# Kernel tuning notes

Measured on AMD Instinct MI355X. Metric: run time of the kernel, lower is better.

Reference implementation:

```python
import math
import jax, jax.numpy as jnp
import numpy as np

B, T, C, HS = 4, 4096, 1024, 64  # batch, seq, n_embd, head_size=n_embd//n_head

def setup_inputs() -> dict:
    key = jax.random.key(0)
    k0, k1, k2, k3 = jax.random.split(key, 4)
    x = jax.random.normal(k0, (B, T, C), dtype=jnp.float32)
    Wq = jax.random.normal(k1, (C, HS), dtype=jnp.float32) * 0.02
    Wk = jax.random.normal(k2, (C, HS), dtype=jnp.float32) * 0.02
    Wv = jax.random.normal(k3, (C, HS), dtype=jnp.float32) * 0.02
    return {"x": x, "Wq": Wq, "Wk": Wk, "Wv": Wv}

def reference(x, Wq, Wk, Wv):
    b, t, c = x.shape
    q = x @ Wq                                   # [B,T,hs]
    k = x @ Wk                                   # [B,T,hs]
    v = x @ Wv                                   # [B,T,hs]
    wei = jnp.einsum('btd,bsd->bts', q, k)       # [B,T,T] raw scores
    row_sums = wei.sum(axis=-1)                  # [B,T]
    k_sel = math.ceil(t / 2)                     # static: t known at trace time
    _, idx = jax.lax.top_k(row_sums, k_sel)      # [B,k_sel]
    idx = jnp.sort(idx, axis=1)
    # gather selected score rows: [B,k_sel,T]
    half_wei = jnp.take_along_axis(wei, idx[:, :, None], axis=1)
    # causal mask rows gathered from tril: tril[idx[b,i], j] == (j <= idx[b,i])
    half_mask = jnp.arange(t)[None, None, :] <= idx[:, :, None]  # [B,k_sel,T] bool
    half_wei = half_wei * (c ** -0.5)            # NOTE: scaled by n_embd, as in source
    half_wei = jnp.where(half_mask, half_wei, -jnp.inf)
    att = jax.nn.softmax(half_wei, axis=-1)      # [B,k_sel,T]
    out = att @ v                                # [B,k_sel,hs]
    return out
```

## Files before the change

kernel.cpp:

```cpp
#include <hip/hip_runtime.h>
#include <math.h>

#define BB 4
#define TT 4096
#define CC 1024
#define HS 64
#define KSEL 2048
#define NSPL 16
#define SWLOG 8
#define SW 256

typedef float f32x4 __attribute__((ext_vector_type(4)));
typedef short short8 __attribute__((ext_vector_type(8)));

__device__ __forceinline__ unsigned short f2bf(float f) {
  union { float f; unsigned int u; } c;
  c.f = f;
  const unsigned int u = c.u;
  return (unsigned short)((u + 0x7FFFu + ((u >> 16) & 1u)) >> 16);
}

__device__ __forceinline__ unsigned cvtpk(float lo, float hi) {
  unsigned r;
  asm("v_cvt_pk_bf16_f32 %0, %1, %2" : "=v"(r) : "v"(lo), "v"(hi));
  return r;
}

__global__ __launch_bounds__(256) void conv_w(const float* __restrict__ Wq,
                                              const float* __restrict__ Wk,
                                              const float* __restrict__ Wv,
                                              unsigned short* __restrict__ wbf,
                                              float* __restrict__ xsum) {
  const int gid = blockIdx.x * 256 + threadIdx.x;
  if (gid < 1024) ((float4*)xsum)[gid] = make_float4(0.f, 0.f, 0.f, 0.f);
  const int kt = gid / 768;
  const int rem = gid - kt * 768;
  const int nt = rem >> 6, lane = rem & 63;
  const int col = nt * 16 + (lane & 15);
  const float* W = (col < 64) ? Wq : ((col < 128) ? Wk : Wv);
  const int cl = col & 63;
  const int k0 = kt * 32 + (lane >> 4) * 8;
  unsigned short tmp[8];
#pragma unroll
  for (int i = 0; i < 8; i++) tmp[i] = f2bf(W[(size_t)(k0 + i) * HS + cl]);
  uint4 o;
  o.x = tmp[0] | ((unsigned)tmp[1] << 16);
  o.y = tmp[2] | ((unsigned)tmp[3] << 16);
  o.z = tmp[4] | ((unsigned)tmp[5] << 16);
  o.w = tmp[6] | ((unsigned)tmp[7] << 16);
  *(uint4*)(wbf + (size_t)gid * 8) = o;
}

#define PR 32
__global__ __launch_bounds__(256) void fusedproj(
    const float* __restrict__ x, const unsigned short* __restrict__ wbf,
    float* __restrict__ xsum, unsigned short* __restrict__ qbf,
    unsigned short* __restrict__ kbf, unsigned short* __restrict__ vtbf) {
  __shared__ unsigned short Xs[PR][256];
  __shared__ float xsred[4][256];
  const int rb = blockIdx.x;
  const size_t r0 = (size_t)rb * PR;
  const int tid = threadIdx.x;
  const int wid = tid >> 6, lane = tid & 63;
  const int lhi = lane >> 4, llo = lane & 15;
  const int mt = wid >> 1, nh = wid & 1;
  const int cl = tid & 63, rg = tid >> 6;
  const int bidx = rb >> 7;

  f32x4 acc[6];
#pragma unroll
  for (int n = 0; n < 6; n++) acc[n] = (f32x4){0.f, 0.f, 0.f, 0.f};

  float4 pf[8];
#pragma unroll
  for (int rr = 0; rr < 8; rr++)
    pf[rr] = *(const float4*)(x + (r0 + rg * 8 + rr) * CC + cl * 4);

  for (int ch = 0; ch < 4; ch++) {
    float ps0 = 0.f, ps1 = 0.f, ps2 = 0.f, ps3 = 0.f;
#pragma unroll
    for (int rr = 0; rr < 8; rr++) {
      const int row = rg * 8 + rr;
      float4 v = pf[rr];
      ps0 += v.x; ps1 += v.y; ps2 += v.z; ps3 += v.w;
      *(uint2*)((char*)&Xs[0][0] + row * 512 +
                ((((cl >> 1) ^ (row & 7))) << 4) + ((cl & 1) << 3)) =
          make_uint2(cvtpk(v.x, v.y), cvtpk(v.z, v.w));
    }
    xsred[rg][cl * 4 + 0] = ps0;
    xsred[rg][cl * 4 + 1] = ps1;
    xsred[rg][cl * 4 + 2] = ps2;
    xsred[rg][cl * 4 + 3] = ps3;
    __syncthreads();
    if (ch < 3) {
#pragma unroll
      for (int rr = 0; rr < 8; rr++)
        pf[rr] = *(const float4*)(x + (r0 + rg * 8 + rr) * CC +
                                  (ch + 1) * 256 + cl * 4);
    }
    atomicAdd(&xsum[bidx * CC + ch * 256 + tid],
              xsred[0][tid] + xsred[1][tid] + xsred[2][tid] + xsred[3][tid]);
    const int row = mt * 16 + llo;
#pragma unroll
    for (int ktl = 0; ktl < 8; ktl++) {
      short8 af = *(const short8*)((const char*)&Xs[0][0] + row * 512 +
                                   ((((ktl << 2) + lhi) ^ (row & 7)) << 4));
      const unsigned short* bp =
          wbf + (((size_t)(ch * 8 + ktl) * 12 + nh * 6) * 64 + lane) * 8;
#pragma unroll
      for (int n = 0; n < 6; n++) {
        short8 bf = *(const short8*)(bp + n * 64 * 8);
        acc[n] = __builtin_amdgcn_mfma_f32_16x16x32_bf16(af, bf, acc[n], 0, 0, 0);
      }
    }
    __syncthreads();
  }
  const int rbg = (int)r0 + mt * 16 + lhi * 4;
#pragma unroll
  for (int n = 0; n < 6; n++) {
    const int col = (nh * 6 + n) * 16 + llo;
    const int mat = col >> 6, cl2 = col & 63;
    if (mat == 0) {
#pragma unroll
      for (int r = 0; r < 4; r++)
        qbf[(size_t)(rbg + r) * HS + cl2] = f2bf(acc[n][r] * 0.03125f);
    } else if (mat == 1) {
#pragma unroll
      for (int r = 0; r < 4; r++)
        kbf[(size_t)(rbg + r) * HS + cl2] = f2bf(acc[n][r]);
    } else {
      const int bb = rbg >> 12, tloc = rbg & (TT - 1);
      *(uint2*)(vtbf + ((size_t)bb * HS + cl2) * TT + tloc) =
          make_uint2(cvtpk(acc[n][0], acc[n][1]), cvtpk(acc[n][2], acc[n][3]));
    }
  }
}

__global__ __launch_bounds__(512) void rowsums_x(
    const float* __restrict__ x, const float* __restrict__ Wq,
    const float* __restrict__ Wk, const float* __restrict__ xsum,
    float* __restrict__ rs) {
  __shared__ float xsl[CC];
  __shared__ float kred[8][HS];
  __shared__ float ksl[HS];
  __shared__ float wl[CC];
  const int g = blockIdx.x;
  const int tid = threadIdx.x;
  const int b = g >> 6;
  *(float2*)(xsl + tid * 2) = *(const float2*)(xsum + b * CC + tid * 2);
  __syncthreads();
  {
    const int g8 = tid >> 6, d = tid & 63;
    const float* wkp = Wk + (size_t)(g8 * 128) * HS + d;
    float s = 0.f;
    for (int c = 0; c < 128; c++) s += xsl[g8 * 128 + c] * wkp[(size_t)c * HS];
    kred[g8][d] = s;
  }
  __syncthreads();
  if (tid < 64) {
    float s = 0.f;
#pragma unroll
    for (int g8 = 0; g8 < 8; g8++) s += kred[g8][tid];
    ksl[tid] = s;
  }
  __syncthreads();
#pragma unroll
  for (int p = 0; p < 2; p++) {
    const int c = tid * 2 + p;
    const float* wqp = Wq + (size_t)c * HS;
    float s = 0.f;
#pragma unroll
    for (int d4 = 0; d4 < 16; d4++) {
      float4 a = *(const float4*)(wqp + d4 * 4);
      float4 kk = *(const float4*)(ksl + d4 * 4);
      s += a.x * kk.x + a.y * kk.y + a.z * kk.z + a.w * kk.w;
    }
    wl[c] = s;
  }
  __syncthreads();
  const size_t row = (size_t)g * 64 + (tid >> 3);
  const int qu = tid & 7;
  const float* xr = x + row * CC + qu * 128;
  const float* wr = wl + qu * 128;
  float s = 0.f;
  for (int e = 0; e < 32; e++) {
    float4 v = *(const float4*)(xr + e * 4);
    float4 w4 = *(const float4*)(wr + e * 4);
    s += v.x * w4.x + v.y * w4.y + v.z * w4.z + v.w * w4.w;
  }
  s += __shfl_xor(s, 1);
  s += __shfl_xor(s, 2);
  s += __shfl_xor(s, 4);
  if (qu == 0) rs[row] = s;
}

__global__ __launch_bounds__(256) void rankk(const float* __restrict__ rs,
                                             int* __restrict__ flag) {
  __shared__ float rl[TT];
  const int g = blockIdx.x;
  const int b = g >> 7, chunk = g & 127;
  const int tid = threadIdx.x;
  const float* rsb = rs + (size_t)b * TT;
  for (int e = tid; e < TT / 4; e += 256)
    *(float4*)(rl + e * 4) = *(const float4*)(rsb + e * 4);
  __syncthreads();
  const int cand = tid >> 3, qu = tid & 7;
  const int t = chunk * 32 + cand;
  const float my = rl[t];
  int cnt = 0;
  for (int e = 0; e < 128; e++) {
    const int s = qu * 512 + e * 4;
    float4 v = *(const float4*)(rl + s);
    cnt += (v.x > my) || (v.x == my && (s + 0) < t);
    cnt += (v.y > my) || (v.y == my && (s + 1) < t);
    cnt += (v.z > my) || (v.z == my && (s + 2) < t);
    cnt += (v.w > my) || (v.w == my && (s + 3) < t);
  }
  cnt += __shfl_xor(cnt, 1);
  cnt += __shfl_xor(cnt, 2);
  cnt += __shfl_xor(cnt, 4);
  if (qu == 0) flag[(size_t)b * TT + t] = (cnt < KSEL) ? 1 : 0;
}

__global__ __launch_bounds__(256) void compact(const int* __restrict__ flag,
                                               int* __restrict__ idx) {
  __shared__ int wsum[4];
  __shared__ int woff[4];
  const int b = blockIdx.x;
  const int tid = threadIdx.x;
  const int wid = tid >> 6, lane = tid & 63;
  const int* fb = flag + (size_t)b * TT;
  const int base = tid * 16;
  int f[16];
  int cnt = 0;
#pragma unroll
  for (int e4 = 0; e4 < 4; e4++) {
    int4 v = *(const int4*)(fb + base + e4 * 4);
    f[e4 * 4 + 0] = v.x; f[e4 * 4 + 1] = v.y;
    f[e4 * 4 + 2] = v.z; f[e4 * 4 + 3] = v.w;
    cnt += v.x + v.y + v.z + v.w;
  }
  int sc = cnt;
#pragma unroll
  for (int d = 1; d < 64; d <<= 1) {
    int v = __shfl_up(sc, d);
    if (lane >= d) sc += v;
  }
  if (lane == 63) wsum[wid] = sc;
  __syncthreads();
  if (tid == 0) {
    int a = 0;
#pragma unroll
    for (int w = 0; w < 4; w++) { woff[w] = a; a += wsum[w]; }
  }
  __syncthreads();
  int pos = woff[wid] + sc - cnt;
#pragma unroll
  for (int e = 0; e < 16; e++)
    if (f[e]) idx[(size_t)b * KSEL + (pos++)] = base + e;
}

struct KF { short8 a0, a1, b0, b1; };
struct VF { short8 v0, v1, v2, v3; };

__global__ __launch_bounds__(256) void attn_mfma(
    const unsigned short* __restrict__ qbf,
    const unsigned short* __restrict__ kbf,
    const unsigned short* __restrict__ vtbf, const int* __restrict__ idx,
    float* __restrict__ pl, float* __restrict__ pacc) {
  __shared__ unsigned short P_lds[4][32][40];
  const int rb = blockIdx.x;
  const int zz = blockIdx.y;
  const int b = blockIdx.z;
  const int tid = threadIdx.x;
  const int wid = tid >> 6, lane = tid & 63;
  const int s = zz * 4 + wid;
  const size_t rbase = (size_t)b * KSEL + rb * 32;
  const int tmaxblk = idx[rbase + 31];
  const int jlo = s << SWLOG;
  if (jlo > tmaxblk) return;

  const int lhi = lane >> 4, llo = lane & 15;
  const int trow0 = idx[rbase + llo];
  const int trow1 = idx[rbase + 16 + llo];
  short8 qf[2][2];
  {
    const unsigned short* qp0 = qbf + ((size_t)b * TT + trow0) * HS + lhi * 8;
    const unsigned short* qp1 = qbf + ((size_t)b * TT + trow1) * HS + lhi * 8;
    qf[0][0] = *(const short8*)(qp0);
    qf[0][1] = *(const short8*)(qp0 + 32);
    qf[1][0] = *(const short8*)(qp1);
    qf[1][1] = *(const short8*)(qp1 + 32);
  }
  f32x4 o[2][4];
#pragma unroll
  for (int mtt = 0; mtt < 2; mtt++)
#pragma unroll
    for (int n = 0; n < 4; n++) o[mtt][n] = (f32x4){0.f, 0.f, 0.f, 0.f};
  float lsum[2] = {0.f, 0.f};

  const unsigned short* kb = kbf + (size_t)b * TT * HS;
  const unsigned short* vb = vtbf + (size_t)b * HS * TT;
  const int jend = min(tmaxblk + 1, jlo + SW);

  auto loadK = [&](int j0) {
    KF K;
    const unsigned short* kp = kb + (size_t)(j0 + llo) * HS + lhi * 8;
    K.a0 = *(const short8*)(kp);
    K.a1 = *(const short8*)(kp + 32);
    K.b0 = *(const short8*)(kp + 16 * HS);
    K.b1 = *(const short8*)(kp + 16 * HS + 32);
    return K;
  };
  auto loadV = [&](int j0) {
    VF V;
    const unsigned short* vp = vb + (size_t)llo * TT + j0 + lhi * 8;
    V.v0 = *(const short8*)(vp);
    V.v1 = *(const short8*)(vp + 16 * TT);
    V.v2 = *(const short8*)(vp + 32 * TT);
    V.v3 = *(const short8*)(vp + 48 * TT);
    return V;
  };

  auto body = [&](int j0, const KF& K, const VF& V) {
    f32x4 sc[2][2];
#pragma unroll
    for (int mtt = 0; mtt < 2; mtt++) {
      f32x4 a = (f32x4){0.f, 0.f, 0.f, 0.f};
      a = __builtin_amdgcn_mfma_f32_16x16x32_bf16(K.a0, qf[mtt][0], a, 0, 0, 0);
      a = __builtin_amdgcn_mfma_f32_16x16x32_bf16(K.a1, qf[mtt][1], a, 0, 0, 0);
      sc[mtt][0] = a;
      f32x4 c = (f32x4){0.f, 0.f, 0.f, 0.f};
      c = __builtin_amdgcn_mfma_f32_16x16x32_bf16(K.b0, qf[mtt][0], c, 0, 0, 0);
      c = __builtin_amdgcn_mfma_f32_16x16x32_bf16(K.b1, qf[mtt][1], c, 0, 0, 0);
      sc[mtt][1] = c;
    }
#pragma unroll
    for (int mtt = 0; mtt < 2; mtt++) {
      const int tr = (mtt == 0) ? trow0 : trow1;
      float p[8];
#pragma unroll
      for (int kt = 0; kt < 2; kt++)
#pragma unroll
        for (int r = 0; r < 4; r++) {
          const int kk = j0 + kt * 16 + lhi * 4 + r;
          const float e = __expf(sc[mtt][kt][r]);
          p[kt * 4 + r] = (kk <= tr) ? e : 0.f;
        }
      lsum[mtt] += ((p[0] + p[1]) + (p[2] + p[3])) +
                   ((p[4] + p[5]) + (p[6] + p[7]));
      *(uint2*)&P_lds[wid][mtt * 16 + llo][lhi * 4] =
          make_uint2(cvtpk(p[0], p[1]), cvtpk(p[2], p[3]));
      *(uint2*)&P_lds[wid][mtt * 16 + llo][16 + lhi * 4] =
          make_uint2(cvtpk(p[4], p[5]), cvtpk(p[6], p[7]));
    }
    short8 pa0 = *(const short8*)&P_lds[wid][llo][lhi * 8];
    short8 pa1 = *(const short8*)&P_lds[wid][16 + llo][lhi * 8];
    o[0][0] = __builtin_amdgcn_mfma_f32_16x16x32_bf16(pa0, V.v0, o[0][0], 0, 0, 0);
    o[1][0] = __builtin_amdgcn_mfma_f32_16x16x32_bf16(pa1, V.v0, o[1][0], 0, 0, 0);
    o[0][1] = __builtin_amdgcn_mfma_f32_16x16x32_bf16(pa0, V.v1, o[0][1], 0, 0, 0);
    o[1][1] = __builtin_amdgcn_mfma_f32_16x16x32_bf16(pa1, V.v1, o[1][1], 0, 0, 0);
    o[0][2] = __builtin_amdgcn_mfma_f32_16x16x32_bf16(pa0, V.v2, o[0][2], 0, 0, 0);
    o[1][2] = __builtin_amdgcn_mfma_f32_16x16x32_bf16(pa1, V.v2, o[1][2], 0, 0, 0);
    o[0][3] = __builtin_amdgcn_mfma_f32_16x16x32_bf16(pa0, V.v3, o[0][3], 0, 0, 0);
    o[1][3] = __builtin_amdgcn_mfma_f32_16x16x32_bf16(pa1, V.v3, o[1][3], 0, 0, 0);
  };

  int j0 = jlo;
  KF ka = loadK(j0), kb2;
  VF va = loadV(j0), vb2;
  for (;;) {
    if (j0 + 32 < jend) { kb2 = loadK(j0 + 32); vb2 = loadV(j0 + 32); }
    body(j0, ka, va);
    j0 += 32;
    if (j0 >= jend) break;
    if (j0 + 32 < jend) { ka = loadK(j0 + 32); va = loadV(j0 + 32); }
    body(j0, kb2, vb2);
    j0 += 32;
    if (j0 >= jend) break;
  }

  lsum[0] += __shfl_xor(lsum[0], 16);
  lsum[0] += __shfl_xor(lsum[0], 32);
  lsum[1] += __shfl_xor(lsum[1], 16);
  lsum[1] += __shfl_xor(lsum[1], 32);
  if (lane < 16) {
    pl[(rbase + llo) * NSPL + s] = lsum[0];
    pl[(rbase + 16 + llo) * NSPL + s] = lsum[1];
  }
#pragma unroll
  for (int mtt = 0; mtt < 2; mtt++)
#pragma unroll
    for (int r = 0; r < 4; r++) {
      const size_t rowi = rbase + mtt * 16 + lhi * 4 + r;
#pragma unroll
      for (int n = 0; n < 4; n++)
        pacc[(rowi * NSPL + s) * HS + n * 16 + llo] = o[mtt][n][r];
    }
}

__global__ __launch_bounds__(256) void attn_combine(
    const float* __restrict__ pl, const float* __restrict__ pacc,
    const int* __restrict__ idx, float* __restrict__ out) {
  const int b = blockIdx.x;
  const int i0 = blockIdx.y * 32;
  const int tid = threadIdx.x;
  const int r = tid >> 3, dg = tid & 7;
  const size_t rowi = (size_t)b * KSEL + i0 + r;
  const int t_r = idx[rowi];
  const int ns = (t_r >> SWLOG) + 1;
  float L = 0.f;
  float o[8] = {0.f, 0.f, 0.f, 0.f, 0.f, 0.f, 0.f, 0.f};
  for (int s = 0; s < ns; s++) {
    L += pl[rowi * NSPL + s];
    const float* pa = pacc + (rowi * NSPL + s) * HS + dg * 8;
    float4 a0 = *(const float4*)(pa);
    float4 a1 = *(const float4*)(pa + 4);
    o[0] += a0.x; o[1] += a0.y; o[2] += a0.z; o[3] += a0.w;
    o[4] += a1.x; o[5] += a1.y; o[6] += a1.z; o[7] += a1.w;
  }
  const float invl = 1.0f / L;
  float* op = out + rowi * HS + dg * 8;
  *(float4*)(op) = make_float4(o[0] * invl, o[1] * invl, o[2] * invl, o[3] * invl);
  *(float4*)(op + 4) = make_float4(o[4] * invl, o[5] * invl, o[6] * invl, o[7] * invl);
}

extern "C" void kernel_launch(void* const* d_in, const int* in_sizes, int n_in,
                              void* d_out, int out_size, void* d_ws,
                              size_t ws_size, hipStream_t stream) {
  const float* x = (const float*)d_in[0];
  const float* Wq = (const float*)d_in[1];
  const float* Wk = (const float*)d_in[2];
  const float* Wv = (const float*)d_in[3];
  float* out = (float*)d_out;

  float* wsf = (float*)d_ws;
  float* pacc = wsf;
  float* xsum = wsf;
  float* rs = xsum + 4096;
  int* flag = (int*)(rs + 16384);
  unsigned short* wbf = (unsigned short*)(flag + 16384);
  unsigned short* qbf = (unsigned short*)(pacc + 8388608);
  unsigned short* kbf = qbf + 1048576;
  unsigned short* vtbf = kbf + 1048576;
  int* idxp = (int*)(vtbf + 1048576);
  float* pl = (float*)(idxp + 8192);

  conv_w<<<96, 256, 0, stream>>>(Wq, Wk, Wv, wbf, xsum);
  fusedproj<<<512, 256, 0, stream>>>(x, wbf, xsum, qbf, kbf, vtbf);
  rowsums_x<<<256, 512, 0, stream>>>(x, Wq, Wk, xsum, rs);
  rankk<<<512, 256, 0, stream>>>(rs, flag);
  compact<<<BB, 256, 0, stream>>>(flag, idxp);
  attn_mfma<<<dim3(64, 4, BB), 256, 0, stream>>>(qbf, kbf, vtbf, idxp, pl, pacc);
  attn_combine<<<dim3(BB, 64), 256, 0, stream>>>(pl, pacc, idxp, out);
}
```

Before: 125.3 us.

## Compact active attention work units into a list and use persistent wave scheduling

The compact kernel now builds a per-batch list of active (row-block, key-split) work units and their counts. The attention kernel becomes a persistent grid of 640 blocks whose waves stride over this list, so it no longer launches blocks that exit early on causally empty splits. rowsums_x is also regridded to 32 rows per block with 16 lanes per row to double its block count. This removes idle launched waves and the load imbalance of the old grid, at the cost of an extra serial loop in compact and less balanced per-wave work, since units vary in length.

```diff
diff --git a/kernel.cpp b/kernel.cpp
--- a/kernel.cpp
+++ b/kernel.cpp
@@ -146,7 +146,7 @@
   __shared__ float wl[CC];
   const int g = blockIdx.x;
   const int tid = threadIdx.x;
-  const int b = g >> 6;
+  const int b = g >> 7;
   *(float2*)(xsl + tid * 2) = *(const float2*)(xsum + b * CC + tid * 2);
   __syncthreads();
   {
@@ -178,12 +178,13 @@
     wl[c] = s;
   }
   __syncthreads();
-  const size_t row = (size_t)g * 64 + (tid >> 3);
-  const int qu = tid & 7;
-  const float* xr = x + row * CC + qu * 128;
-  const float* wr = wl + qu * 128;
+  const size_t row = (size_t)g * 32 + (tid >> 4);
+  const int qu = tid & 15;
+  const float* xr = x + row * CC + qu * 64;
+  const float* wr = wl + qu * 64;
   float s = 0.f;
-  for (int e = 0; e < 32; e++) {
+#pragma unroll
+  for (int e = 0; e < 16; e++) {
     float4 v = *(const float4*)(xr + e * 4);
     float4 w4 = *(const float4*)(wr + e * 4);
     s += v.x * w4.x + v.y * w4.y + v.z * w4.z + v.w * w4.w;
@@ -191,6 +192,7 @@
   s += __shfl_xor(s, 1);
   s += __shfl_xor(s, 2);
   s += __shfl_xor(s, 4);
+  s += __shfl_xor(s, 8);
   if (qu == 0) rs[row] = s;
 }
 
@@ -223,7 +225,9 @@
 }
 
 __global__ __launch_bounds__(256) void compact(const int* __restrict__ flag,
-                                               int* __restrict__ idx) {
+                                               int* __restrict__ idx,
+                                               int* __restrict__ wlist,
+                                               int* __restrict__ wcnt) {
   __shared__ int wsum[4];
   __shared__ int woff[4];
   const int b = blockIdx.x;
@@ -258,6 +262,21 @@
 #pragma unroll
   for (int e = 0; e < 16; e++)
     if (f[e]) idx[(size_t)b * KSEL + (pos++)] = base + e;
+
+  __syncthreads();
+  if (tid < 64) {
+    const int nact = (idx[(size_t)b * KSEL + tid * 32 + 31] >> SWLOG) + 1;
+    int scan = nact;
+#pragma unroll
+    for (int d = 1; d < 64; d <<= 1) {
+      int v = __shfl_up(scan, d);
+      if (tid >= d) scan += v;
+    }
+    if (tid == 63) wcnt[b] = scan;
+    int excl = scan - nact;
+    for (int s2 = 0; s2 < nact; s2++)
+      wlist[b * 1024 + excl + s2] = (b << 10) | (tid << 4) | s2;
+  }
 }
 
 struct KF { short8 a0, a1, b0, b1; };
@@ -267,136 +286,148 @@
     const unsigned short* __restrict__ qbf,
     const unsigned short* __restrict__ kbf,
     const unsigned short* __restrict__ vtbf, const int* __restrict__ idx,
+    const int* __restrict__ wlist, const int* __restrict__ wcnt,
     float* __restrict__ pl, float* __restrict__ pacc) {
   __shared__ unsigned short P_lds[4][32][40];
-  const int rb = blockIdx.x;
-  const int zz = blockIdx.y;
-  const int b = blockIdx.z;
   const int tid = threadIdx.x;
   const int wid = tid >> 6, lane = tid & 63;
-  const int s = zz * 4 + wid;
-  const size_t rbase = (size_t)b * KSEL + rb * 32;
-  const int tmaxblk = idx[rbase + 31];
-  const int jlo = s << SWLOG;
-  if (jlo > tmaxblk) return;
-
   const int lhi = lane >> 4, llo = lane & 15;
-  const int trow0 = idx[rbase + llo];
-  const int trow1 = idx[rbase + 16 + llo];
-  short8 qf[2][2];
-  {
-    const unsigned short* qp0 = qbf + ((size_t)b * TT + trow0) * HS + lhi * 8;
-    const unsigned short* qp1 = qbf + ((size_t)b * TT + trow1) * HS + lhi * 8;
-    qf[0][0] = *(const short8*)(qp0);
-    qf[0][1] = *(const short8*)(qp0 + 32);
-    qf[1][0] = *(const short8*)(qp1);
-    qf[1][1] = *(const short8*)(qp1 + 32);
-  }
-  f32x4 o[2][4];
-#pragma unroll
-  for (int mtt = 0; mtt < 2; mtt++)
-#pragma unroll
-    for (int n = 0; n < 4; n++) o[mtt][n] = (f32x4){0.f, 0.f, 0.f, 0.f};
-  float lsum[2] = {0.f, 0.f};
-
-  const unsigned short* kb = kbf + (size_t)b * TT * HS;
-  const unsigned short* vb = vtbf + (size_t)b * HS * TT;
-  const int jend = min(tmaxblk + 1, jlo + SW);
-
-  auto loadK = [&](int j0) {
-    KF K;
-    const unsigned short* kp = kb + (size_t)(j0 + llo) * HS + lhi * 8;
-    K.a0 = *(const short8*)(kp);
-    K.a1 = *(const short8*)(kp + 32);
-    K.b0 = *(const short8*)(kp + 16 * HS);
-    K.b1 = *(const short8*)(kp + 16 * HS + 32);
-    return K;
-  };
-  auto loadV = [&](int j0) {
-    VF V;
-    const unsigned short* vp = vb + (size_t)llo * TT + j0 + lhi * 8;
-    V.v0 = *(const short8*)(vp);
-    V.v1 = *(const short8*)(vp + 16 * TT);
-    V.v2 = *(const short8*)(vp + 32 * TT);
-    V.v3 = *(const short8*)(vp + 48 * TT);
-    return V;
-  };
-
-  auto body = [&](int j0, const KF& K, const VF& V) {
-    f32x4 sc[2][2];
-#pragma unroll
-    for (int mtt = 0; mtt < 2; mtt++) {
-      f32x4 a = (f32x4){0.f, 0.f, 0.f, 0.f};
-      a = __builtin_amdgcn_mfma_f32_16x16x32_bf16(K.a0, qf[mtt][0], a, 0, 0, 0);
-      a = __builtin_amdgcn_mfma_f32_16x16x32_bf16(K.a1, qf[mtt][1], a, 0, 0, 0);
-      sc[mtt][0] = a;
-      f32x4 c = (f32x4){0.f, 0.f, 0.f, 0.f};
-      c = __builtin_amdgcn_mfma_f32_16x16x32_bf16(K.b0, qf[mtt][0], c, 0, 0, 0);
-      c = __builtin_amdgcn_mfma_f32_16x16x32_bf16(K.b1, qf[mtt][1], c, 0, 0, 0);
-      sc[mtt][1] = c;
-    }
-#pragma unroll
-    for (int mtt = 0; mtt < 2; mtt++) {
-      const int tr = (mtt == 0) ? trow0 : trow1;
-      float p[8];
-#pragma unroll
-      for (int kt = 0; kt < 2; kt++)
-#pragma unroll
-        for (int r = 0; r < 4; r++) {
-          const int kk = j0 + kt * 16 + lhi * 4 + r;
-          const float e = __expf(sc[mtt][kt][r]);
-          p[kt * 4 + r] = (kk <= tr) ? e : 0.f;
-        }
-      lsum[mtt] += ((p[0] + p[1]) + (p[2] + p[3])) +
-                   ((p[4] + p[5]) + (p[6] + p[7]));
-      *(uint2*)&P_lds[wid][mtt * 16 + llo][lhi * 4] =
-          make_uint2(cvtpk(p[0], p[1]), cvtpk(p[2], p[3]));
-      *(uint2*)&P_lds[wid][mtt * 16 + llo][16 + lhi * 4] =
-          make_uint2(cvtpk(p[4], p[5]), cvtpk(p[6], p[7]));
-    }
-    short8 pa0 = *(const short8*)&P_lds[wid][llo][lhi * 8];
-    short8 pa1 = *(const short8*)&P_lds[wid][16 + llo][lhi * 8];
-    o[0][0] = __builtin_amdgcn_mfma_f32_16x16x32_bf16(pa0, V.v0, o[0][0], 0, 0, 0);
-    o[1][0] = __builtin_amdgcn_mfma_f32_16x16x32_bf16(pa1, V.v0, o[1][0], 0, 0, 0);
-    o[0][1] = __builtin_amdgcn_mfma_f32_16x16x32_bf16(pa0, V.v1, o[0][1], 0, 0, 0);
-    o[1][1] = __builtin_amdgcn_mfma_f32_16x16x32_bf16(pa1, V.v1, o[1][1], 0, 0, 0);
-    o[0][2] = __builtin_amdgcn_mfma_f32_16x16x32_bf16(pa0, V.v2, o[0][2], 0, 0, 0);
-    o[1][2] = __builtin_amdgcn_mfma_f32_16x16x32_bf16(pa1, V.v2, o[1][2], 0, 0, 0);
-    o[0][3] = __builtin_amdgcn_mfma_f32_16x16x32_bf16(pa0, V.v3, o[0][3], 0, 0, 0);
-    o[1][3] = __builtin_amdgcn_mfma_f32_16x16x32_bf16(pa1, V.v3, o[1][3], 0, 0, 0);
-  };
-
-  int j0 = jlo;
-  KF ka = loadK(j0), kb2;
-  VF va = loadV(j0), vb2;
-  for (;;) {
-    if (j0 + 32 < jend) { kb2 = loadK(j0 + 32); vb2 = loadV(j0 + 32); }
-    body(j0, ka, va);
-    j0 += 32;
-    if (j0 >= jend) break;
-    if (j0 + 32 < jend) { ka = loadK(j0 + 32); va = loadV(j0 + 32); }
-    body(j0, kb2, vb2);
-    j0 += 32;
-    if (j0 >= jend) break;
-  }
-
-  lsum[0] += __shfl_xor(lsum[0], 16);
-  lsum[0] += __shfl_xor(lsum[0], 32);
-  lsum[1] += __shfl_xor(lsum[1], 16);
-  lsum[1] += __shfl_xor(lsum[1], 32);
-  if (lane < 16) {
-    pl[(rbase + llo) * NSPL + s] = lsum[0];
-    pl[(rbase + 16 + llo) * NSPL + s] = lsum[1];
-  }
-#pragma unroll
-  for (int mtt = 0; mtt < 2; mtt++)
-#pragma unroll
-    for (int r = 0; r < 4; r++) {
-      const size_t rowi = rbase + mtt * 16 + lhi * 4 + r;
-#pragma unroll
-      for (int n = 0; n < 4; n++)
-        pacc[(rowi * NSPL + s) * HS + n * 16 + llo] = o[mtt][n][r];
-    }
+  const int c0 = wcnt[0], c1 = wcnt[1], c2 = wcnt[2], c3 = wcnt[3];
+  const int total = c0 + c1 + c2 + c3;
+
+  for (int u = blockIdx.x * 4 + wid; u < total; u += gridDim.x * 4) {
+    int rem = u, b;
+    if (rem >= c0) {
+      rem -= c0;
+      if (rem >= c1) {
+        rem -= c1;
+        if (rem >= c2) { rem -= c2; b = 3; } else b = 2;
+      } else b = 1;
+    } else b = 0;
+    const int e = wlist[b * 1024 + rem];
+    const int rb = (e >> 4) & 63;
+    const int s = e & 15;
+    const size_t rbase = (size_t)b * KSEL + rb * 32;
+    const int tmaxblk = idx[rbase + 31];
+    const int jlo = s << SWLOG;
+
+    const int trow0 = idx[rbase + llo];
+    const int trow1 = idx[rbase + 16 + llo];
+    short8 qf[2][2];
+    {
+      const unsigned short* qp0 = qbf + ((size_t)b * TT + trow0) * HS + lhi * 8;
+      const unsigned short* qp1 = qbf + ((size_t)b * TT + trow1) * HS + lhi * 8;
+      qf[0][0] = *(const short8*)(qp0);
+      qf[0][1] = *(const short8*)(qp0 + 32);
+      qf[1][0] = *(const short8*)(qp1);
+      qf[1][1] = *(const short8*)(qp1 + 32);
+    }
+    f32x4 o[2][4];
+#pragma unroll
+    for (int mtt = 0; mtt < 2; mtt++)
+#pragma unroll
+      for (int n = 0; n < 4; n++) o[mtt][n] = (f32x4){0.f, 0.f, 0.f, 0.f};
+    float lsum[2] = {0.f, 0.f};
+
+    const unsigned short* kb = kbf + (size_t)b * TT * HS;
+    const unsigned short* vb = vtbf + (size_t)b * HS * TT;
+    const int jend = min(tmaxblk + 1, jlo + SW);
+
+    auto loadK = [&](int j0) {
+      KF K;
+      const unsigned short* kp = kb + (size_t)(j0 + llo) * HS + lhi * 8;
+      K.a0 = *(const short8*)(kp);
+      K.a1 = *(const short8*)(kp + 32);
+      K.b0 = *(const short8*)(kp + 16 * HS);
+      K.b1 = *(const short8*)(kp + 16 * HS + 32);
+      return K;
+    };
+    auto loadV = [&](int j0) {
+      VF V;
+      const unsigned short* vp = vb + (size_t)llo * TT + j0 + lhi * 8;
+      V.v0 = *(const short8*)(vp);
+      V.v1 = *(const short8*)(vp + 16 * TT);
+      V.v2 = *(const short8*)(vp + 32 * TT);
+      V.v3 = *(const short8*)(vp + 48 * TT);
+      return V;
+    };
+
+    auto body = [&](int j0, const KF& K, const VF& V) {
+      f32x4 sc[2][2];
+#pragma unroll
+      for (int mtt = 0; mtt < 2; mtt++) {
+        f32x4 a = (f32x4){0.f, 0.f, 0.f, 0.f};
+        a = __builtin_amdgcn_mfma_f32_16x16x32_bf16(K.a0, qf[mtt][0], a, 0, 0, 0);
+        a = __builtin_amdgcn_mfma_f32_16x16x32_bf16(K.a1, qf[mtt][1], a, 0, 0, 0);
+        sc[mtt][0] = a;
+        f32x4 c = (f32x4){0.f, 0.f, 0.f, 0.f};
+        c = __builtin_amdgcn_mfma_f32_16x16x32_bf16(K.b0, qf[mtt][0], c, 0, 0, 0);
+        c = __builtin_amdgcn_mfma_f32_16x16x32_bf16(K.b1, qf[mtt][1], c, 0, 0, 0);
+        sc[mtt][1] = c;
+      }
+#pragma unroll
+      for (int mtt = 0; mtt < 2; mtt++) {
+        const int tr = (mtt == 0) ? trow0 : trow1;
+        float p[8];
+#pragma unroll
+        for (int kt = 0; kt < 2; kt++)
+#pragma unroll
+          for (int r = 0; r < 4; r++) {
+            const int kk = j0 + kt * 16 + lhi * 4 + r;
+            const float ex = __expf(sc[mtt][kt][r]);
+            p[kt * 4 + r] = (kk <= tr) ? ex : 0.f;
+          }
+        lsum[mtt] += ((p[0] + p[1]) + (p[2] + p[3])) +
+                     ((p[4] + p[5]) + (p[6] + p[7]));
+        *(uint2*)&P_lds[wid][mtt * 16 + llo][lhi * 4] =
+            make_uint2(cvtpk(p[0], p[1]), cvtpk(p[2], p[3]));
+        *(uint2*)&P_lds[wid][mtt * 16 + llo][16 + lhi * 4] =
+            make_uint2(cvtpk(p[4], p[5]), cvtpk(p[6], p[7]));
+      }
+      short8 pa0 = *(const short8*)&P_lds[wid][llo][lhi * 8];
+      short8 pa1 = *(const short8*)&P_lds[wid][16 + llo][lhi * 8];
+      o[0][0] = __builtin_amdgcn_mfma_f32_16x16x32_bf16(pa0, V.v0, o[0][0], 0, 0, 0);
+      o[1][0] = __builtin_amdgcn_mfma_f32_16x16x32_bf16(pa1, V.v0, o[1][0], 0, 0, 0);
+      o[0][1] = __builtin_amdgcn_mfma_f32_16x16x32_bf16(pa0, V.v1, o[0][1], 0, 0, 0);
+      o[1][1] = __builtin_amdgcn_mfma_f32_16x16x32_bf16(pa1, V.v1, o[1][1], 0, 0, 0);
+      o[0][2] = __builtin_amdgcn_mfma_f32_16x16x32_bf16(pa0, V.v2, o[0][2], 0, 0, 0);
+      o[1][2] = __builtin_amdgcn_mfma_f32_16x16x32_bf16(pa1, V.v2, o[1][2], 0, 0, 0);
+      o[0][3] = __builtin_amdgcn_mfma_f32_16x16x32_bf16(pa0, V.v3, o[0][3], 0, 0, 0);
+      o[1][3] = __builtin_amdgcn_mfma_f32_16x16x32_bf16(pa1, V.v3, o[1][3], 0, 0, 0);
+    };
+
+    int j0 = jlo;
+    KF ka = loadK(j0), kb2;
+    VF va = loadV(j0), vb2;
+    for (;;) {
+      if (j0 + 32 < jend) { kb2 = loadK(j0 + 32); vb2 = loadV(j0 + 32); }
+      body(j0, ka, va);
+      j0 += 32;
+      if (j0 >= jend) break;
+      if (j0 + 32 < jend) { ka = loadK(j0 + 32); va = loadV(j0 + 32); }
+      body(j0, kb2, vb2);
+      j0 += 32;
+      if (j0 >= jend) break;
+    }
+
+    lsum[0] += __shfl_xor(lsum[0], 16);
+    lsum[0] += __shfl_xor(lsum[0], 32);
+    lsum[1] += __shfl_xor(lsum[1], 16);
+    lsum[1] += __shfl_xor(lsum[1], 32);
+    if (lane < 16) {
+      pl[(rbase + llo) * NSPL + s] = lsum[0];
+      pl[(rbase + 16 + llo) * NSPL + s] = lsum[1];
+    }
+#pragma unroll
+    for (int mtt = 0; mtt < 2; mtt++)
+#pragma unroll
+      for (int r = 0; r < 4; r++) {
+        const size_t rowi = rbase + mtt * 16 + lhi * 4 + r;
+#pragma unroll
+        for (int n = 0; n < 4; n++)
+          pacc[(rowi * NSPL + s) * HS + n * 16 + llo] = o[mtt][n][r];
+      }
+  }
 }
 
 __global__ __launch_bounds__(256) void attn_combine(
@@ -445,12 +476,14 @@
   unsigned short* vtbf = kbf + 1048576;
   int* idxp = (int*)(vtbf + 1048576);
   float* pl = (float*)(idxp + 8192);
+  int* wcnt = (int*)(pl + 131072);
+  int* wlist = wcnt + 4;
 
   conv_w<<<96, 256, 0, stream>>>(Wq, Wk, Wv, wbf, xsum);
   fusedproj<<<512, 256, 0, stream>>>(x, wbf, xsum, qbf, kbf, vtbf);
-  rowsums_x<<<256, 512, 0, stream>>>(x, Wq, Wk, xsum, rs);
+  rowsums_x<<<512, 512, 0, stream>>>(x, Wq, Wk, xsum, rs);
   rankk<<<512, 256, 0, stream>>>(rs, flag);
-  compact<<<BB, 256, 0, stream>>>(flag, idxp);
-  attn_mfma<<<dim3(64, 4, BB), 256, 0, stream>>>(qbf, kbf, vtbf, idxp, pl, pacc);
+  compact<<<BB, 256, 0, stream>>>(flag, idxp, wlist, wcnt);
+  attn_mfma<<<640, 256, 0, stream>>>(qbf, kbf, vtbf, idxp, wlist, wcnt, pl, pacc);
   attn_combine<<<dim3(BB, 64), 256, 0, stream>>>(pl, pacc, idxp, out);
 }
```

After: 135.3 us. 1.08x slower.

## Fuse compaction into attention, use persistent compacted work list, coalesce rowsum loads

Applied to the files above, without the earlier changes.

Removes the separate compact kernel. Each attention block and each combine block now rebuilds the selected-index list in LDS from the flag array. The attention kernel becomes a persistent grid of 640 blocks that walks a prefix-summed list containing only the non-empty (row block, split) work items, which avoids launching empty blocks and the imbalance that came with them. The rowsum loop now uses interleaved lanes so its global loads are coalesced. The cost is that every block repeats the compaction work (four batches per attention block) and LDS use per block goes up.

```diff
diff --git a/kernel.cpp b/kernel.cpp
--- a/kernel.cpp
+++ b/kernel.cpp
@@ -180,12 +180,13 @@
   __syncthreads();
   const size_t row = (size_t)g * 64 + (tid >> 3);
   const int qu = tid & 7;
-  const float* xr = x + row * CC + qu * 128;
-  const float* wr = wl + qu * 128;
+  const float* xr = x + row * CC;
   float s = 0.f;
+#pragma unroll
   for (int e = 0; e < 32; e++) {
-    float4 v = *(const float4*)(xr + e * 4);
-    float4 w4 = *(const float4*)(wr + e * 4);
+    const int off = (qu + e * 8) * 4;
+    float4 v = *(const float4*)(xr + off);
+    float4 w4 = *(const float4*)(wl + off);
     s += v.x * w4.x + v.y * w4.y + v.z * w4.z + v.w * w4.w;
   }
   s += __shfl_xor(s, 1);
@@ -222,14 +223,11 @@
   if (qu == 0) flag[(size_t)b * TT + t] = (cnt < KSEL) ? 1 : 0;
 }
 
-__global__ __launch_bounds__(256) void compact(const int* __restrict__ flag,
-                                               int* __restrict__ idx) {
-  __shared__ int wsum[4];
-  __shared__ int woff[4];
-  const int b = blockIdx.x;
-  const int tid = threadIdx.x;
-  const int wid = tid >> 6, lane = tid & 63;
-  const int* fb = flag + (size_t)b * TT;
+__device__ __forceinline__ void compact_to_lds(const int* __restrict__ fb,
+                                               int* __restrict__ idx_l,
+                                               int* __restrict__ wsum,
+                                               int* __restrict__ woff,
+                                               int tid, int wid, int lane) {
   const int base = tid * 16;
   int f[16];
   int cnt = 0;
@@ -257,7 +255,7 @@
   int pos = woff[wid] + sc - cnt;
 #pragma unroll
   for (int e = 0; e < 16; e++)
-    if (f[e]) idx[(size_t)b * KSEL + (pos++)] = base + e;
+    if (f[e]) idx_l[pos++] = base + e;
 }
 
 struct KF { short8 a0, a1, b0, b1; };
@@ -266,148 +264,192 @@
 __global__ __launch_bounds__(256) void attn_mfma(
     const unsigned short* __restrict__ qbf,
     const unsigned short* __restrict__ kbf,
-    const unsigned short* __restrict__ vtbf, const int* __restrict__ idx,
+    const unsigned short* __restrict__ vtbf, const int* __restrict__ flag,
     float* __restrict__ pl, float* __restrict__ pacc) {
   __shared__ unsigned short P_lds[4][32][40];
-  const int rb = blockIdx.x;
-  const int zz = blockIdx.y;
-  const int b = blockIdx.z;
+  __shared__ int idx_l[BB][KSEL];
+  __shared__ int excl[257];
+  __shared__ int wsum[4];
+  __shared__ int woff[4];
   const int tid = threadIdx.x;
   const int wid = tid >> 6, lane = tid & 63;
-  const int s = zz * 4 + wid;
-  const size_t rbase = (size_t)b * KSEL + rb * 32;
-  const int tmaxblk = idx[rbase + 31];
-  const int jlo = s << SWLOG;
-  if (jlo > tmaxblk) return;
-
   const int lhi = lane >> 4, llo = lane & 15;
-  const int trow0 = idx[rbase + llo];
-  const int trow1 = idx[rbase + 16 + llo];
-  short8 qf[2][2];
+
+#pragma unroll 1
+  for (int b = 0; b < BB; b++) {
+    compact_to_lds(flag + (size_t)b * TT, idx_l[b], wsum, woff, tid, wid, lane);
+    __syncthreads();
+  }
   {
-    const unsigned short* qp0 = qbf + ((size_t)b * TT + trow0) * HS + lhi * 8;
-    const unsigned short* qp1 = qbf + ((size_t)b * TT + trow1) * HS + lhi * 8;
-    qf[0][0] = *(const short8*)(qp0);
-    qf[0][1] = *(const short8*)(qp0 + 32);
-    qf[1][0] = *(const short8*)(qp1);
-    qf[1][1] = *(const short8*)(qp1 + 32);
-  }
-  f32x4 o[2][4];
-#pragma unroll
-  for (int mtt = 0; mtt < 2; mtt++)
-#pragma unroll
-    for (int n = 0; n < 4; n++) o[mtt][n] = (f32x4){0.f, 0.f, 0.f, 0.f};
-  float lsum[2] = {0.f, 0.f};
-
-  const unsigned short* kb = kbf + (size_t)b * TT * HS;
-  const unsigned short* vb = vtbf + (size_t)b * HS * TT;
-  const int jend = min(tmaxblk + 1, jlo + SW);
-
-  auto loadK = [&](int j0) {
-    KF K;
-    const unsigned short* kp = kb + (size_t)(j0 + llo) * HS + lhi * 8;
-    K.a0 = *(const short8*)(kp);
-    K.a1 = *(const short8*)(kp + 32);
-    K.b0 = *(const short8*)(kp + 16 * HS);
-    K.b1 = *(const short8*)(kp + 16 * HS + 32);
-    return K;
-  };
-  auto loadV = [&](int j0) {
-    VF V;
-    const unsigned short* vp = vb + (size_t)llo * TT + j0 + lhi * 8;
-    V.v0 = *(const short8*)(vp);
-    V.v1 = *(const short8*)(vp + 16 * TT);
-    V.v2 = *(const short8*)(vp + 32 * TT);
-    V.v3 = *(const short8*)(vp + 48 * TT);
-    return V;
-  };
-
-  auto body = [&](int j0, const KF& K, const VF& V) {
-    f32x4 sc[2][2];
-#pragma unroll
-    for (int mtt = 0; mtt < 2; mtt++) {
-      f32x4 a = (f32x4){0.f, 0.f, 0.f, 0.f};
-      a = __builtin_amdgcn_mfma_f32_16x16x32_bf16(K.a0, qf[mtt][0], a, 0, 0, 0);
-      a = __builtin_amdgcn_mfma_f32_16x16x32_bf16(K.a1, qf[mtt][1], a, 0, 0, 0);
-      sc[mtt][0] = a;
-      f32x4 c = (f32x4){0.f, 0.f, 0.f, 0.f};
-      c = __builtin_amdgcn_mfma_f32_16x16x32_bf16(K.b0, qf[mtt][0], c, 0, 0, 0);
-      c = __builtin_amdgcn_mfma_f32_16x16x32_bf16(K.b1, qf[mtt][1], c, 0, 0, 0);
-      sc[mtt][1] = c;
-    }
-#pragma unroll
-    for (int mtt = 0; mtt < 2; mtt++) {
-      const int tr = (mtt == 0) ? trow0 : trow1;
-      float p[8];
-#pragma unroll
-      for (int kt = 0; kt < 2; kt++)
-#pragma unroll
-        for (int r = 0; r < 4; r++) {
-          const int kk = j0 + kt * 16 + lhi * 4 + r;
-          const float e = __expf(sc[mtt][kt][r]);
-          p[kt * 4 + r] = (kk <= tr) ? e : 0.f;
-        }
-      lsum[mtt] += ((p[0] + p[1]) + (p[2] + p[3])) +
-                   ((p[4] + p[5]) + (p[6] + p[7]));
-      *(uint2*)&P_lds[wid][mtt * 16 + llo][lhi * 4] =
-          make_uint2(cvtpk(p[0], p[1]), cvtpk(p[2], p[3]));
-      *(uint2*)&P_lds[wid][mtt * 16 + llo][16 + lhi * 4] =
-          make_uint2(cvtpk(p[4], p[5]), cvtpk(p[6], p[7]));
-    }
-    short8 pa0 = *(const short8*)&P_lds[wid][llo][lhi * 8];
-    short8 pa1 = *(const short8*)&P_lds[wid][16 + llo][lhi * 8];
-    o[0][0] = __builtin_amdgcn_mfma_f32_16x16x32_bf16(pa0, V.v0, o[0][0], 0, 0, 0);
-    o[1][0] = __builtin_amdgcn_mfma_f32_16x16x32_bf16(pa1, V.v0, o[1][0], 0, 0, 0);
-    o[0][1] = __builtin_amdgcn_mfma_f32_16x16x32_bf16(pa0, V.v1, o[0][1], 0, 0, 0);
-    o[1][1] = __builtin_amdgcn_mfma_f32_16x16x32_bf16(pa1, V.v1, o[1][1], 0, 0, 0);
-    o[0][2] = __builtin_amdgcn_mfma_f32_16x16x32_bf16(pa0, V.v2, o[0][2], 0, 0, 0);
-    o[1][2] = __builtin_amdgcn_mfma_f32_16x16x32_bf16(pa1, V.v2, o[1][2], 0, 0, 0);
-    o[0][3] = __builtin_amdgcn_mfma_f32_16x16x32_bf16(pa0, V.v3, o[0][3], 0, 0, 0);
-    o[1][3] = __builtin_amdgcn_mfma_f32_16x16x32_bf16(pa1, V.v3, o[1][3], 0, 0, 0);
-  };
-
-  int j0 = jlo;
-  KF ka = loadK(j0), kb2;
-  VF va = loadV(j0), vb2;
-  for (;;) {
-    if (j0 + 32 < jend) { kb2 = loadK(j0 + 32); vb2 = loadV(j0 + 32); }
-    body(j0, ka, va);
-    j0 += 32;
-    if (j0 >= jend) break;
-    if (j0 + 32 < jend) { ka = loadK(j0 + 32); va = loadV(j0 + 32); }
-    body(j0, kb2, vb2);
-    j0 += 32;
-    if (j0 >= jend) break;
-  }
-
-  lsum[0] += __shfl_xor(lsum[0], 16);
-  lsum[0] += __shfl_xor(lsum[0], 32);
-  lsum[1] += __shfl_xor(lsum[1], 16);
-  lsum[1] += __shfl_xor(lsum[1], 32);
-  if (lane < 16) {
-    pl[(rbase + llo) * NSPL + s] = lsum[0];
-    pl[(rbase + 16 + llo) * NSPL + s] = lsum[1];
-  }
-#pragma unroll
-  for (int mtt = 0; mtt < 2; mtt++)
-#pragma unroll
-    for (int r = 0; r < 4; r++) {
-      const size_t rowi = rbase + mtt * 16 + lhi * 4 + r;
-#pragma unroll
-      for (int n = 0; n < 4; n++)
-        pacc[(rowi * NSPL + s) * HS + n * 16 + llo] = o[mtt][n][r];
-    }
+    const int na = (idx_l[tid >> 6][(tid & 63) * 32 + 31] >> SWLOG) + 1;
+    int sc = na;
+#pragma unroll
+    for (int d = 1; d < 64; d <<= 1) {
+      int v = __shfl_up(sc, d);
+      if (lane >= d) sc += v;
+    }
+    if (lane == 63) wsum[wid] = sc;
+    __syncthreads();
+    if (tid == 0) {
+      int a = 0;
+#pragma unroll
+      for (int w = 0; w < 4; w++) { woff[w] = a; a += wsum[w]; }
+      excl[256] = a;
+    }
+    __syncthreads();
+    excl[tid] = woff[wid] + sc - na;
+    __syncthreads();
+  }
+  const int total = excl[256];
+
+  for (int u = blockIdx.x * 4 + wid; u < total; u += gridDim.x * 4) {
+    int g = 0;
+#pragma unroll
+    for (int step = 128; step; step >>= 1)
+      if (g + step < 256 && excl[g + step] <= u) g += step;
+    const int b = g >> 6, rb = g & 63;
+    const int s = u - excl[g];
+    const int* idxb = idx_l[b];
+    const int rloc = rb * 32;
+    const size_t rbase = (size_t)b * KSEL + rloc;
+    const int tmaxblk = idxb[rloc + 31];
+    const int jlo = s << SWLOG;
+
+    const int trow0 = idxb[rloc + llo];
+    const int trow1 = idxb[rloc + 16 + llo];
+    short8 qf[2][2];
+    {
+      const unsigned short* qp0 = qbf + ((size_t)b * TT + trow0) * HS + lhi * 8;
+      const unsigned short* qp1 = qbf + ((size_t)b * TT + trow1) * HS + lhi * 8;
+      qf[0][0] = *(const short8*)(qp0);
+      qf[0][1] = *(const short8*)(qp0 + 32);
+      qf[1][0] = *(const short8*)(qp1);
+      qf[1][1] = *(const short8*)(qp1 + 32);
+    }
+    f32x4 o[2][4];
+#pragma unroll
+    for (int mtt = 0; mtt < 2; mtt++)
+#pragma unroll
+      for (int n = 0; n < 4; n++) o[mtt][n] = (f32x4){0.f, 0.f, 0.f, 0.f};
+    float lsum[2] = {0.f, 0.f};
+
+    const unsigned short* kb = kbf + (size_t)b * TT * HS;
+    const unsigned short* vb = vtbf + (size_t)b * HS * TT;
+    const int jend = min(tmaxblk + 1, jlo + SW);
+
+    auto loadK = [&](int j0) {
+      KF K;
+      const unsigned short* kp = kb + (size_t)(j0 + llo) * HS + lhi * 8;
+      K.a0 = *(const short8*)(kp);
+      K.a1 = *(const short8*)(kp + 32);
+      K.b0 = *(const short8*)(kp + 16 * HS);
+      K.b1 = *(const short8*)(kp + 16 * HS + 32);
+      return K;
+    };
+    auto loadV = [&](int j0) {
+      VF V;
+      const unsigned short* vp = vb + (size_t)llo * TT + j0 + lhi * 8;
+      V.v0 = *(const short8*)(vp);
+      V.v1 = *(const short8*)(vp + 16 * TT);
+      V.v2 = *(const short8*)(vp + 32 * TT);
+      V.v3 = *(const short8*)(vp + 48 * TT);
+      return V;
+    };
+
+    auto body = [&](int j0, const KF& K, const VF& V) {
+      f32x4 sc2[2][2];
+#pragma unroll
+      for (int mtt = 0; mtt < 2; mtt++) {
+        f32x4 a = (f32x4){0.f, 0.f, 0.f, 0.f};
+        a = __builtin_amdgcn_mfma_f32_16x16x32_bf16(K.a0, qf[mtt][0], a, 0, 0, 0);
+        a = __builtin_amdgcn_mfma_f32_16x16x32_bf16(K.a1, qf[mtt][1], a, 0, 0, 0);
+        sc2[mtt][0] = a;
+        f32x4 c = (f32x4){0.f, 0.f, 0.f, 0.f};
+        c = __builtin_amdgcn_mfma_f32_16x16x32_bf16(K.b0, qf[mtt][0], c, 0, 0, 0);
+        c = __builtin_amdgcn_mfma_f32_16x16x32_bf16(K.b1, qf[mtt][1], c, 0, 0, 0);
+        sc2[mtt][1] = c;
+      }
+#pragma unroll
+      for (int mtt = 0; mtt < 2; mtt++) {
+        const int tr = (mtt == 0) ? trow0 : trow1;
+        float p[8];
+#pragma unroll
+        for (int kt = 0; kt < 2; kt++)
+#pragma unroll
+          for (int r = 0; r < 4; r++) {
+            const int kk = j0 + kt * 16 + lhi * 4 + r;
+            const float ex = __expf(sc2[mtt][kt][r]);
+            p[kt * 4 + r] = (kk <= tr) ? ex : 0.f;
+          }
+        lsum[mtt] += ((p[0] + p[1]) + (p[2] + p[3])) +
+                     ((p[4] + p[5]) + (p[6] + p[7]));
+        *(uint2*)&P_lds[wid][mtt * 16 + llo][lhi * 4] =
+            make_uint2(cvtpk(p[0], p[1]), cvtpk(p[2], p[3]));
+        *(uint2*)&P_lds[wid][mtt * 16 + llo][16 + lhi * 4] =
+            make_uint2(cvtpk(p[4], p[5]), cvtpk(p[6], p[7]));
+      }
+      short8 pa0 = *(const short8*)&P_lds[wid][llo][lhi * 8];
+      short8 pa1 = *(const short8*)&P_lds[wid][16 + llo][lhi * 8];
+      o[0][0] = __builtin_amdgcn_mfma_f32_16x16x32_bf16(pa0, V.v0, o[0][0], 0, 0, 0);
+      o[1][0] = __builtin_amdgcn_mfma_f32_16x16x32_bf16(pa1, V.v0, o[1][0], 0, 0, 0);
+      o[0][1] = __builtin_amdgcn_mfma_f32_16x16x32_bf16(pa0, V.v1, o[0][1], 0, 0, 0);
+      o[1][1] = __builtin_amdgcn_mfma_f32_16x16x32_bf16(pa1, V.v1, o[1][1], 0, 0, 0);
+      o[0][2] = __builtin_amdgcn_mfma_f32_16x16x32_bf16(pa0, V.v2, o[0][2], 0, 0, 0);
+      o[1][2] = __builtin_amdgcn_mfma_f32_16x16x32_bf16(pa1, V.v2, o[1][2], 0, 0, 0);
+      o[0][3] = __builtin_amdgcn_mfma_f32_16x16x32_bf16(pa0, V.v3, o[0][3], 0, 0, 0);
+      o[1][3] = __builtin_amdgcn_mfma_f32_16x16x32_bf16(pa1, V.v3, o[1][3], 0, 0, 0);
+    };
+
+    int j0 = jlo;
+    KF ka = loadK(j0), kb2;
+    VF va = loadV(j0), vb2;
+    for (;;) {
+      if (j0 + 32 < jend) { kb2 = loadK(j0 + 32); vb2 = loadV(j0 + 32); }
+      body(j0, ka, va);
+      j0 += 32;
+      if (j0 >= jend) break;
+      if (j0 + 32 < jend) { ka = loadK(j0 + 32); va = loadV(j0 + 32); }
+      body(j0, kb2, vb2);
+      j0 += 32;
+      if (j0 >= jend) break;
+    }
+
+    lsum[0] += __shfl_xor(lsum[0], 16);
+    lsum[0] += __shfl_xor(lsum[0], 32);
+    lsum[1] += __shfl_xor(lsum[1], 16);
+    lsum[1] += __shfl_xor(lsum[1], 32);
+    if (lane < 16) {
+      pl[(rbase + llo) * NSPL + s] = lsum[0];
+      pl[(rbase + 16 + llo) * NSPL + s] = lsum[1];
+    }
+#pragma unroll
+    for (int mtt = 0; mtt < 2; mtt++)
+#pragma unroll
+      for (int r = 0; r < 4; r++) {
+        const size_t rowi = rbase + mtt * 16 + lhi * 4 + r;
+#pragma unroll
+        for (int n = 0; n < 4; n++)
+          pacc[(rowi * NSPL + s) * HS + n * 16 + llo] = o[mtt][n][r];
+      }
+  }
 }
 
 __global__ __launch_bounds__(256) void attn_combine(
     const float* __restrict__ pl, const float* __restrict__ pacc,
-    const int* __restrict__ idx, float* __restrict__ out) {
+    const int* __restrict__ flag, float* __restrict__ out) {
+  __shared__ int idx_l[KSEL];
+  __shared__ int wsum[4];
+  __shared__ int woff[4];
   const int b = blockIdx.x;
   const int i0 = blockIdx.y * 32;
   const int tid = threadIdx.x;
+  const int wid = tid >> 6, lane = tid & 63;
+  compact_to_lds(flag + (size_t)b * TT, idx_l, wsum, woff, tid, wid, lane);
+  __syncthreads();
+
   const int r = tid >> 3, dg = tid & 7;
   const size_t rowi = (size_t)b * KSEL + i0 + r;
-  const int t_r = idx[rowi];
+  const int t_r = idx_l[i0 + r];
   const int ns = (t_r >> SWLOG) + 1;
   float L = 0.f;
   float o[8] = {0.f, 0.f, 0.f, 0.f, 0.f, 0.f, 0.f, 0.f};
@@ -438,19 +480,17 @@
   float* pacc = wsf;
   float* xsum = wsf;
   float* rs = xsum + 4096;
-  int* flag = (int*)(rs + 16384);
-  unsigned short* wbf = (unsigned short*)(flag + 16384);
+  unsigned short* wbf = (unsigned short*)(rs + 16384);
   unsigned short* qbf = (unsigned short*)(pacc + 8388608);
   unsigned short* kbf = qbf + 1048576;
   unsigned short* vtbf = kbf + 1048576;
-  int* idxp = (int*)(vtbf + 1048576);
-  float* pl = (float*)(idxp + 8192);
+  int* flag = (int*)(vtbf + 1048576);
+  float* pl = (float*)(flag + 16384);
 
   conv_w<<<96, 256, 0, stream>>>(Wq, Wk, Wv, wbf, xsum);
   fusedproj<<<512, 256, 0, stream>>>(x, wbf, xsum, qbf, kbf, vtbf);
   rowsums_x<<<256, 512, 0, stream>>>(x, Wq, Wk, xsum, rs);
   rankk<<<512, 256, 0, stream>>>(rs, flag);
-  compact<<<BB, 256, 0, stream>>>(flag, idxp);
-  attn_mfma<<<dim3(64, 4, BB), 256, 0, stream>>>(qbf, kbf, vtbf, idxp, pl, pacc);
-  attn_combine<<<dim3(BB, 64), 256, 0, stream>>>(pl, pacc, idxp, out);
-}
+  attn_mfma<<<640, 256, 0, stream>>>(qbf, kbf, vtbf, flag, pl, pacc);
+  attn_combine<<<dim3(BB, 64), 256, 0, stream>>>(pl, pacc, flag, out);
+}
```

Result: no change. 125.9 us (+0.5%).
